# Kernel optimization log

Hardware: AMD Instinct MI355X
Metric: run time of the kernel (lower is better)

The kernel has to match this reference:

```python
import jax, jax.numpy as jnp
import numpy as np

N, E, C, A, F = 10000, 128000, 128, 10, 8
LDIMS = (1, 3, 5)  # 0e, 1o, 2e spherical-harmonic block sizes
NPATH = len(LDIMS)


def setup_inputs() -> dict:
    key = jax.random.key(0)
    ks = jax.random.split(key, 16)
    rn = lambda k, s, sc=1.0: jax.random.normal(k, s, dtype=jnp.float32) * sc
    inp = {
        "node_attrs": rn(ks[0], (N, A)),
        "node_feats": rn(ks[1], (N, C)),
        "edge_attrs_real": rn(ks[2], (E, 9)),
        "edge_attrs_imag": rn(ks[3], (E, 9)),
        "edge_feats": jax.random.uniform(ks[4], (E, F), dtype=jnp.float32),
        "edge_index": jax.random.randint(ks[5], (2, E), 0, N, dtype=jnp.int32),
        # learned parameters (e3nn 1/sqrt(fan_in) normalization folded into init)
        "W_up": rn(ks[6], (C, C), 1.0 / np.sqrt(C)),            # o3.Linear on 128x0e
        "W_skip": rn(ks[7], (C, A, C), 1.0 / np.sqrt(C * A)),    # FullyConnectedTensorProduct
        "W_mlp1": rn(ks[8], (F, 64), 1.0 / np.sqrt(F)),
        "W_mlp2": rn(ks[9], (64, 64), 1.0 / 8.0),
        "W_mlp3": rn(ks[10], (64, 64), 1.0 / 8.0),
        "W_mlp4": rn(ks[11], (64, NPATH * C), 1.0 / 8.0),        # -> conv_tp.weight_numel = 384
        "W_lin0": rn(ks[12], (C, C), 1.0 / np.sqrt(C)),          # o3.Linear per-l blocks
        "W_lin1": rn(ks[13], (C, C), 1.0 / np.sqrt(C)),
        "W_lin2": rn(ks[14], (C, C), 1.0 / np.sqrt(C)),
    }
    return inp


def _conv_tp(x, y, w):
    """scalar(128x0e) x sh(0e+1o+2e) uvu tensor product with per-edge weights.
    x: [E,C] sender scalars, y: [E,9] edge sh, w: [E,NPATH,C] -> [E, C*9] irreps_mid layout."""
    outs, off = [], 0
    for l, d in enumerate(LDIMS):
        yl = y[:, off:off + d]                      # [E,d]
        off += d
        xw = x * w[:, l]                            # [E,C]
        outs.append((xw[:, :, None] * yl[:, None, :]).reshape(-1, C * d))
    return jnp.concatenate(outs, axis=-1)           # [E, C*(1+3+5)]


def _linear_irreps(m, Ws):
    """o3.Linear mixing channels within each l block. m: [N, C*9] -> [N, C, 9]."""
    outs, off = [], 0
    for l, d in enumerate(LDIMS):
        blk = m[:, off:off + C * d].reshape(-1, C, d)  # [N,C,d]
        off += C * d
        outs.append(jnp.einsum('num,uk->nkm', blk, Ws[l]))
    return jnp.concatenate(outs, axis=-1)              # [N,C,9] (reshape_irreps layout)


def reference(node_attrs, node_feats, edge_attrs_real, edge_attrs_imag, edge_feats,
              edge_index, W_up, W_skip, W_mlp1, W_mlp2, W_mlp3, W_mlp4,
              W_lin0, W_lin1, W_lin2):
    sender, receiver = edge_index[0], edge_index[1]
    # skip connection: FullyConnectedTensorProduct(node_feats 128x0e, node_attrs 10x0e)
    sc = jnp.einsum('nu,nv,uvk->nk', node_feats, node_attrs, W_skip)
    # linear_up
    h = node_feats @ W_up
    # per-edge tensor-product weights from radial MLP (silu hidden layers, linear out)
    t = jax.nn.silu(edge_feats @ W_mlp1)
    t = jax.nn.silu(t @ W_mlp2)
    t = jax.nn.silu(t @ W_mlp3)
    tpw = (t @ W_mlp4).reshape(-1, NPATH, C)
    # gather senders, tensor product for real and imag edge attrs
    xs = h[sender]
    mji_r = _conv_tp(xs, edge_attrs_real, tpw)
    mji_i = _conv_tp(xs, edge_attrs_imag, tpw)
    # scatter-sum to receivers
    msg_r = jax.ops.segment_sum(mji_r, receiver, num_segments=N)
    msg_i = jax.ops.segment_sum(mji_i, receiver, num_segments=N)
    # output linear + reshape_irreps -> [N, C, 9]
    Ws = (W_lin0, W_lin1, W_lin2)
    out_r = _linear_irreps(msg_r, Ws)
    out_i = _linear_irreps(msg_i, Ws)
    return out_r, out_i, sc
```

## Files before the change

kernel.cpp:

```cpp
#include <hip/hip_runtime.h>
#include <hip/hip_bf16.h>

#define N_NODES 10000
#define N_EDGES 128000
#define C_DIM   128

typedef __attribute__((ext_vector_type(8))) short bf16x8;
typedef __attribute__((ext_vector_type(4))) float f32x4;


__device__ __forceinline__ float silu_f(float x) {
  return x / (1.f + __expf(-x));
}

__device__ __forceinline__ unsigned short f2bf(float x) {
  __hip_bfloat16 b = __float2bfloat16(x);
  return *(unsigned short*)&b;
}

__device__ __forceinline__ float bf2f(unsigned short u) {
  __hip_bfloat16 b = *(__hip_bfloat16*)&u;
  return __bfloat162float(b);
}

__device__ __forceinline__ bf16x8 pack8(float4 lo, float4 hi) {
  bf16x8 r;
  r[0] = (short)f2bf(lo.x); r[1] = (short)f2bf(lo.y);
  r[2] = (short)f2bf(lo.z); r[3] = (short)f2bf(lo.w);
  r[4] = (short)f2bf(hi.x); r[5] = (short)f2bf(hi.y);
  r[6] = (short)f2bf(hi.z); r[7] = (short)f2bf(hi.w);
  return r;
}

#define HB_NODES 40
__global__ __launch_bounds__(256) void k_h(const float* __restrict__ feats,
                                           const float* __restrict__ Wup,
                                           float* __restrict__ h) {
  int tid = threadIdx.x;
  int j = tid & 127;
  int par = tid >> 7;
  int n0 = blockIdx.x * HB_NODES;
  float wreg[128];
  #pragma unroll
  for (int k = 0; k < 128; k++) wreg[k] = Wup[k * 128 + j];
  #pragma unroll 2
  for (int i = par; i < HB_NODES; i += 2) {
    int n = __builtin_amdgcn_readfirstlane(n0 + i);
    const float* fr = &feats[n * 128];
    float acc = 0.f;
    #pragma unroll
    for (int k = 0; k < 128; k++) acc += fr[k] * wreg[k];
    h[n * 128 + j] = acc;
  }
}

__global__ void k_wcvt(const float* __restrict__ Wskip,
                       const float* __restrict__ Wl0,
                       const float* __restrict__ Wl1,
                       const float* __restrict__ Wl2,
                       const float* __restrict__ W1, const float* __restrict__ W2,
                       const float* __restrict__ W3, const float* __restrict__ W4,
                       unsigned short* __restrict__ wbT,
                       unsigned short* __restrict__ wlT,
                       unsigned short* __restrict__ w1f, unsigned short* __restrict__ w2f,
                       unsigned short* __restrict__ w3f, unsigned short* __restrict__ w4f) {
  int idx = blockIdx.x * 256 + threadIdx.x;
  if (idx < 163840) {
    int j = idx >> 7, k = idx & 127;
    int u = j / 10, v = j - u * 10;
    wbT[k * 1280 + v * 128 + u] = f2bf(Wskip[idx]);
  } else if (idx < 212992) {
    int t = idx - 163840;
    int l = t >> 14, r = t & 16383;
    int u = r >> 7, k = r & 127;
    const float* W = (l == 0) ? Wl0 : (l == 1) ? Wl1 : Wl2;
    wlT[(l * 128 + k) * 128 + u] = f2bf(W[r]);
  } else if (idx < 215040) {
    int j = idx - 212992;
    int ct = j >> 9, r = j & 511, n = r >> 5, t = r & 31;
    w1f[j] = (t < 8) ? f2bf(W1[t * 64 + ct * 16 + n]) : (unsigned short)0;
  } else if (idx < 219136) {
    int j = idx - 215040;
    int ctks = j >> 9, r = j & 511, n = r >> 5, t = r & 31;
    int ct = ctks >> 1, ks = ctks & 1;
    w2f[j] = f2bf(W2[(ks * 32 + t) * 64 + ct * 16 + n]);
  } else if (idx < 223232) {
    int j = idx - 219136;
    int ctks = j >> 9, r = j & 511, n = r >> 5, t = r & 31;
    int ct = ctks >> 1, ks = ctks & 1;
    w3f[j] = f2bf(W3[(ks * 32 + t) * 64 + ct * 16 + n]);
  } else if (idx < 247808) {
    int j = idx - 223232;
    int ctks = j >> 9, r = j & 511, n = r >> 5, t = r & 31;
    int ct = ctks >> 1, ks = ctks & 1;
    w4f[j] = f2bf(W4[(ks * 32 + t) * 384 + ct * 16 + n]);
  }
}

__global__ __launch_bounds__(256) void k_sc(const float* __restrict__ f,
                                            const float* __restrict__ at,
                                            const unsigned short* __restrict__ wbT,
                                            float* __restrict__ sc_out) {
  int tid = threadIdx.x;
  int w = tid >> 6, lane = tid & 63;
  int l15 = lane & 15, quad = lane >> 4;
  int n0 = blockIdx.x * 32;

  int nrow[2];
  #pragma unroll
  for (int t = 0; t < 2; t++) {
    int n = n0 + 16 * t + l15;
    nrow[t] = (n < N_NODES) ? n : (N_NODES - 1);
  }
  float4 fA[2][4][2];
  #pragma unroll
  for (int t = 0; t < 2; t++)
    #pragma unroll
    for (int ks = 0; ks < 4; ks++) {
      fA[t][ks][0] = *(const float4*)&f[nrow[t] * 128 + ks * 32 + quad * 8];
      fA[t][ks][1] = *(const float4*)&f[nrow[t] * 128 + ks * 32 + quad * 8 + 4];
    }

  f32x4 acc[2][2] = {};
  #pragma unroll 1
  for (int c = 0; c < 10; c++) {
    float av[2];
    #pragma unroll
    for (int t = 0; t < 2; t++) av[t] = at[nrow[t] * 10 + c];
    bf16x8 af[2][4];
    #pragma unroll
    for (int t = 0; t < 2; t++)
      #pragma unroll
      for (int ks = 0; ks < 4; ks++) {
        float4 lo = fA[t][ks][0], hi = fA[t][ks][1];
        lo.x *= av[t]; lo.y *= av[t]; lo.z *= av[t]; lo.w *= av[t];
        hi.x *= av[t]; hi.y *= av[t]; hi.z *= av[t]; hi.w *= av[t];
        af[t][ks] = pack8(lo, hi);
      }
    #pragma unroll
    for (int kt = 0; kt < 2; kt++) {
      int kcol = w * 32 + kt * 16 + l15;
      #pragma unroll
      for (int ks = 0; ks < 4; ks++) {
        bf16x8 bf = *(const bf16x8*)&wbT[kcol * 1280 + c * 128 + ks * 32 + quad * 8];
        #pragma unroll
        for (int t = 0; t < 2; t++)
          acc[t][kt] = __builtin_amdgcn_mfma_f32_16x16x32_bf16(af[t][ks], bf,
                                                               acc[t][kt], 0, 0, 0);
      }
    }
  }
  #pragma unroll
  for (int t = 0; t < 2; t++)
    #pragma unroll
    for (int kt = 0; kt < 2; kt++) {
      int kcol = w * 32 + kt * 16 + l15;
      #pragma unroll
      for (int reg = 0; reg < 4; reg++) {
        int n = n0 + 16 * t + quad * 4 + reg;
        if (n < N_NODES)
          __builtin_nontemporal_store(acc[t][kt][reg], &sc_out[n * 128 + kcol]);
      }
    }
}

__global__ __launch_bounds__(256) void k_mlp(const float* __restrict__ ef,
                                             const int* __restrict__ order,
                                             const unsigned short* __restrict__ w1f,
                                             const unsigned short* __restrict__ w2f,
                                             const unsigned short* __restrict__ w3f,
                                             const unsigned short* __restrict__ w4f,
                                             unsigned short* __restrict__ tpw) {
  __shared__ unsigned short sA[128][72];
  __shared__ unsigned short sB[128][72];
  int tid = threadIdx.x;
  int w = tid >> 6, lane = tid & 63;
  int l15 = lane & 15, quad = lane >> 4;
  int e0 = blockIdx.x * 128;
  int fragoff = l15 * 32 + quad * 8;
  int rb = w * 32;

  {
    bf16x8 af[2];
    #pragma unroll
    for (int rt = 0; rt < 2; rt++) {
      bf16x8 a = {};
      if (quad == 0) {
        int pos = e0 + rb + rt * 16 + l15;
        int e = order[pos];
        float4 lo = *(const float4*)&ef[e * 8];
        float4 hi = *(const float4*)&ef[e * 8 + 4];
        a = pack8(lo, hi);
      }
      af[rt] = a;
    }
    f32x4 ac[2][4] = {};
    #pragma unroll
    for (int ct = 0; ct < 4; ct++) {
      bf16x8 b = *(const bf16x8*)&w1f[ct * 512 + fragoff];
      ac[0][ct] = __builtin_amdgcn_mfma_f32_16x16x32_bf16(af[0], b, ac[0][ct], 0, 0, 0);
      ac[1][ct] = __builtin_amdgcn_mfma_f32_16x16x32_bf16(af[1], b, ac[1][ct], 0, 0, 0);
    }
    #pragma unroll
    for (int rt = 0; rt < 2; rt++)
      #pragma unroll
      for (int ct = 0; ct < 4; ct++)
        #pragma unroll
        for (int reg = 0; reg < 4; reg++)
          sA[rb + rt * 16 + quad * 4 + reg][ct * 16 + l15] =
              f2bf(silu_f(ac[rt][ct][reg]));
  }
  asm volatile("" ::: "memory");

  #pragma unroll 1
  for (int layer = 0; layer < 2; layer++) {
    unsigned short (*src)[72] = (layer == 0) ? sA : sB;
    unsigned short (*dst)[72] = (layer == 0) ? sB : sA;
    const unsigned short* wf = (layer == 0) ? w2f : w3f;
    bf16x8 a2[2][2];
    #pragma unroll
    for (int rt = 0; rt < 2; rt++)
      #pragma unroll
      for (int ks = 0; ks < 2; ks++)
        a2[rt][ks] = *(const bf16x8*)&src[rb + rt * 16 + l15][ks * 32 + quad * 8];
    f32x4 ac[2][4] = {};
    #pragma unroll
    for (int ct = 0; ct < 4; ct++)
      #pragma unroll
      for (int ks = 0; ks < 2; ks++) {
        bf16x8 b = *(const bf16x8*)&wf[(ct * 2 + ks) * 512 + fragoff];
        ac[0][ct] = __builtin_amdgcn_mfma_f32_16x16x32_bf16(a2[0][ks], b, ac[0][ct], 0, 0, 0);
        ac[1][ct] = __builtin_amdgcn_mfma_f32_16x16x32_bf16(a2[1][ks], b, ac[1][ct], 0, 0, 0);
      }
    #pragma unroll
    for (int rt = 0; rt < 2; rt++)
      #pragma unroll
      for (int ct = 0; ct < 4; ct++)
        #pragma unroll
        for (int reg = 0; reg < 4; reg++)
          dst[rb + rt * 16 + quad * 4 + reg][ct * 16 + l15] =
              f2bf(silu_f(ac[rt][ct][reg]));
    asm volatile("" ::: "memory");
  }

  bf16x8 a4[2][2];
  #pragma unroll
  for (int rt = 0; rt < 2; rt++)
    #pragma unroll
    for (int ks = 0; ks < 2; ks++)
      a4[rt][ks] = *(const bf16x8*)&sA[rb + rt * 16 + l15][ks * 32 + quad * 8];

  #pragma unroll 1
  for (int ch = 0; ch < 6; ch++) {
    f32x4 ac[2][4] = {};
    #pragma unroll
    for (int ct = 0; ct < 4; ct++)
      #pragma unroll
      for (int ks = 0; ks < 2; ks++) {
        bf16x8 b = *(const bf16x8*)&w4f[((ch * 4 + ct) * 2 + ks) * 512 + fragoff];
        ac[0][ct] = __builtin_amdgcn_mfma_f32_16x16x32_bf16(a4[0][ks], b, ac[0][ct], 0, 0, 0);
        ac[1][ct] = __builtin_amdgcn_mfma_f32_16x16x32_bf16(a4[1][ks], b, ac[1][ct], 0, 0, 0);
      }
    #pragma unroll
    for (int rt = 0; rt < 2; rt++)
      #pragma unroll
      for (int ct = 0; ct < 4; ct++)
        #pragma unroll
        for (int reg = 0; reg < 4; reg++)
          sB[rb + rt * 16 + quad * 4 + reg][ct * 16 + l15] = f2bf(ac[rt][ct][reg]);
    asm volatile("" ::: "memory");
    #pragma unroll
    for (int v = 0; v < 4; v++) {
      int idx = v * 64 + lane;
      int r = idx >> 3, cg = idx & 7;
      uint4 p = *(const uint4*)&sB[rb + r][cg * 8];
      *(uint4*)&tpw[(size_t)(e0 + rb + r) * 384 + ch * 64 + cg * 8] = p;
    }
    asm volatile("" ::: "memory");
  }
}

__global__ void k_hist(const int* __restrict__ recv, int* __restrict__ counts) {
  int e = blockIdx.x * 256 + threadIdx.x;
  if (e < N_EDGES) atomicAdd(&counts[recv[e]], 1);
}

__global__ __launch_bounds__(1024) void k_scan(const int* __restrict__ counts,
                                               int* __restrict__ offsets,
                                               int* __restrict__ cursor) {
  __shared__ int swave[16];
  int tid = threadIdx.x;
  int lane = tid & 63, w = tid >> 6;
  int base = tid * 10;
  int local[10]; int s = 0;
  #pragma unroll
  for (int i = 0; i < 10; i++) {
    int idx = base + i;
    int c = (idx < N_NODES) ? counts[idx] : 0;
    local[i] = s; s += c;
  }
  int inc = s;
  #pragma unroll
  for (int d = 1; d < 64; d <<= 1) {
    int v = __shfl_up(inc, d, 64);
    if (lane >= d) inc += v;
  }
  if (lane == 63) swave[w] = inc;
  __syncthreads();
  if (w == 0) {
    int t = (lane < 16) ? swave[lane] : 0;
    #pragma unroll
    for (int d = 1; d < 16; d <<= 1) {
      int v = __shfl_up(t, d, 64);
      if (lane >= d) t += v;
    }
    if (lane < 16) swave[lane] = t;
  }
  __syncthreads();
  int wpre = (w > 0) ? swave[w - 1] : 0;
  int pre = wpre + (inc - s);
  #pragma unroll
  for (int i = 0; i < 10; i++) {
    int idx = base + i;
    if (idx < N_NODES) { int o = pre + local[i]; offsets[idx] = o; cursor[idx] = o; }
  }
  if (tid == 1023) offsets[N_NODES] = wpre + inc;
}

__global__ void k_scatter(const int* __restrict__ recv, const int* __restrict__ send,
                          const float* __restrict__ yr, const float* __restrict__ yi,
                          int* __restrict__ cursor, int* __restrict__ order,
                          float* __restrict__ y2, int* __restrict__ ss) {
  int e = blockIdx.x * 256 + threadIdx.x;
  if (e < N_EDGES) {
    int idx = atomicAdd(&cursor[recv[e]], 1);
    order[idx] = e;
    ss[idx] = send[e];
    float* yy = &y2[(size_t)idx * 20];
    #pragma unroll
    for (int m = 0; m < 9; m++) {
      yy[m] = yr[e * 9 + m];
      yy[9 + m] = yi[e * 9 + m];
    }
    yy[18] = 0.f; yy[19] = 0.f;
  }
}

__device__ __forceinline__ void edge_fma(const float* __restrict__ y2, int pos,
                                         float xv, float t0, float t1, float t2,
                                         float* mr, float* mi) {
  const float* yy = &y2[(size_t)pos * 20];
  float4 v0 = *(const float4*)&yy[0];
  float4 v1 = *(const float4*)&yy[4];
  float4 v2 = *(const float4*)&yy[8];
  float4 v3 = *(const float4*)&yy[12];
  float2 v4 = *(const float2*)&yy[16];
  float xw0 = xv * t0, xw1 = xv * t1, xw2 = xv * t2;
  mr[0] += xw0 * v0.x;
  mr[1] += xw1 * v0.y; mr[2] += xw1 * v0.z; mr[3] += xw1 * v0.w;
  mr[4] += xw2 * v1.x; mr[5] += xw2 * v1.y; mr[6] += xw2 * v1.z;
  mr[7] += xw2 * v1.w; mr[8] += xw2 * v2.x;
  mi[0] += xw0 * v2.y;
  mi[1] += xw1 * v2.z; mi[2] += xw1 * v2.w; mi[3] += xw1 * v3.x;
  mi[4] += xw2 * v3.y; mi[5] += xw2 * v3.z; mi[6] += xw2 * v3.w;
  mi[7] += xw2 * v4.x; mi[8] += xw2 * v4.y;
}

__global__ __launch_bounds__(128, 6) void k_gather(
    const float* __restrict__ h, const unsigned short* __restrict__ tpw,
    const float* __restrict__ y2, const int* __restrict__ ss,
    const int* __restrict__ offsets,
    unsigned short* __restrict__ msg) {
  int u = threadIdx.x;
  int n = blockIdx.x;
  float mr[9] = {}, mi[9] = {};
  int e0 = __builtin_amdgcn_readfirstlane(offsets[n]);
  int e1 = __builtin_amdgcn_readfirstlane(offsets[n + 1]);
  int jj = e0;
  for (; jj + 3 < e1; jj += 4) {
    float xv[4], t0[4], t1[4], t2[4];
    #pragma unroll
    for (int q = 0; q < 4; q++) {
      int pos = jj + q;
      int s = ss[pos];
      const unsigned short* tp = &tpw[(size_t)pos * 384 + u];
      t0[q] = bf2f(__builtin_nontemporal_load(tp));
      t1[q] = bf2f(__builtin_nontemporal_load(tp + 128));
      t2[q] = bf2f(__builtin_nontemporal_load(tp + 256));
      xv[q] = h[s * 128 + u];
    }
    #pragma unroll
    for (int q = 0; q < 4; q++)
      edge_fma(y2, jj + q, xv[q], t0[q], t1[q], t2[q], mr, mi);
  }
  for (; jj < e1; jj++) {
    int s = ss[jj];
    const unsigned short* tp = &tpw[(size_t)jj * 384 + u];
    float t0 = bf2f(__builtin_nontemporal_load(tp));
    float t1 = bf2f(__builtin_nontemporal_load(tp + 128));
    float t2 = bf2f(__builtin_nontemporal_load(tp + 256));
    float xv = h[s * 128 + u];
    edge_fma(y2, jj, xv, t0, t1, t2, mr, mi);
  }
  int g = n >> 3, i = n & 7;
  unsigned short* mg = msg + (size_t)g * 144 * 128;
  mg[(i * 2 + 0) * 128 + u] = f2bf(mr[0]);
  mg[(i * 2 + 1) * 128 + u] = f2bf(mi[0]);
  #pragma unroll
  for (int m = 1; m < 4; m++) {
    mg[(16 + i * 6 + (m - 1)) * 128 + u] = f2bf(mr[m]);
    mg[(16 + i * 6 + 3 + (m - 1)) * 128 + u] = f2bf(mi[m]);
  }
  #pragma unroll
  for (int m = 4; m < 9; m++) {
    mg[(64 + i * 10 + (m - 4)) * 128 + u] = f2bf(mr[m]);
    mg[(64 + i * 10 + 5 + (m - 4)) * 128 + u] = f2bf(mi[m]);
  }
}

#define LIN_ROWPAD 1156
__global__ __launch_bounds__(256) void k_lin(const unsigned short* __restrict__ msg,
                                             const unsigned short* __restrict__ wlT,
                                             float* __restrict__ out) {
  __shared__ float so[2 * 8 * LIN_ROWPAD];
  int tid = threadIdx.x;
  int w = tid >> 6, lane = tid & 63;
  int l15 = lane & 15, quad = lane >> 4;
  int g = blockIdx.x;

  bf16x8 bfr[3][2][4];
  #pragma unroll
  for (int l = 0; l < 3; l++)
    #pragma unroll
    for (int kt = 0; kt < 2; kt++)
      #pragma unroll
      for (int ks = 0; ks < 4; ks++) {
        int ncol = w * 32 + kt * 16 + l15;
        bfr[l][kt][ks] = *(const bf16x8*)&wlT[(l * 128 + ncol) * 128 + ks * 32 + quad * 8];
      }

  const unsigned short* mg = msg + (size_t)g * 144 * 128;

  #pragma unroll
  for (int tile = 0; tile < 9; tile++) {
    const int l = (tile == 0) ? 0 : (tile < 4) ? 1 : 2;
    const int rbase = tile * 16;
    bf16x8 af[4];
    #pragma unroll
    for (int ks = 0; ks < 4; ks++)
      af[ks] = *(const bf16x8*)&mg[(rbase + l15) * 128 + ks * 32 + quad * 8];
    f32x4 acc0 = {}, acc1 = {};
    #pragma unroll
    for (int ks = 0; ks < 4; ks++) {
      acc0 = __builtin_amdgcn_mfma_f32_16x16x32_bf16(af[ks], bfr[l][0][ks], acc0, 0, 0, 0);
      acc1 = __builtin_amdgcn_mfma_f32_16x16x32_bf16(af[ks], bfr[l][1][ks], acc1, 0, 0, 0);
    }
    #pragma unroll
    for (int reg = 0; reg < 4; reg++) {
      int r = rbase + quad * 4 + reg;
      int c, ni, m;
      if (tile == 0) { ni = (r & 15) >> 1; c = r & 1; m = 0; }
      else if (tile < 4) {
        int q = r - 16; ni = q / 6; int rem = q - ni * 6;
        c = rem >= 3; m = 1 + rem - (c ? 3 : 0);
      } else {
        int q = r - 64; ni = q / 10; int rem = q - ni * 10;
        c = rem >= 5; m = 4 + rem - (c ? 5 : 0);
      }
      int k0 = w * 32 + l15;
      float* ob = &so[(c * 8 + ni) * LIN_ROWPAD + m];
      ob[(k0)      * 9] = acc0[reg];
      ob[(k0 + 16) * 9] = acc1[reg];
    }
  }
  __syncthreads();
  #pragma unroll
  for (int v = 0; v < 18; v++) {
    int idx = v * 256 + tid;
    int c = idx / 2304;
    int rem = idx - c * 2304;
    int ni = rem / 288;
    int off4 = rem - ni * 288;
    f32x4 p = *(const f32x4*)&so[(c * 8 + ni) * LIN_ROWPAD + off4 * 4];
    f32x4* dst = (f32x4*)&out[(size_t)c * 11520000 + ((size_t)g * 8 + ni) * 1152 +
                              (size_t)off4 * 4];
    __builtin_nontemporal_store(p, dst);
  }
}

extern "C" void kernel_launch(void* const* d_in, const int* in_sizes, int n_in,
                              void* d_out, int out_size, void* d_ws, size_t ws_size,
                              hipStream_t stream) {
  const float* node_attrs = (const float*)d_in[0];
  const float* node_feats = (const float*)d_in[1];
  const float* ear   = (const float*)d_in[2];
  const float* eai   = (const float*)d_in[3];
  const float* ef    = (const float*)d_in[4];
  const int*   eidx  = (const int*)d_in[5];
  const float* Wup   = (const float*)d_in[6];
  const float* Wskip = (const float*)d_in[7];
  const float* W1    = (const float*)d_in[8];
  const float* W2    = (const float*)d_in[9];
  const float* W3    = (const float*)d_in[10];
  const float* W4    = (const float*)d_in[11];
  const float* Wl0   = (const float*)d_in[12];
  const float* Wl1   = (const float*)d_in[13];
  const float* Wl2   = (const float*)d_in[14];
  float* out = (float*)d_out;

  char* ws = (char*)d_ws;
  float*          h       = (float*)ws;
  unsigned short* tpw     = (unsigned short*)(ws + 5120000);
  unsigned short* msg     = (unsigned short*)(ws + 103424000);
  unsigned short* wlT     = (unsigned short*)(ws + 149504000);
  unsigned short* wbT     = (unsigned short*)(ws + 149602304);
  int*            counts  = (int*)(ws + 149929984);
  int*            offsets = (int*)(ws + 149969984);
  int*            cursor  = (int*)(ws + 150010112);
  int*            order   = (int*)(ws + 150050112);
  unsigned short* w1f     = (unsigned short*)(ws + 150562816);
  unsigned short* w2f     = (unsigned short*)(ws + 150566912);
  unsigned short* w3f     = (unsigned short*)(ws + 150575104);
  unsigned short* w4f     = (unsigned short*)(ws + 150583296);

  float* y2 = (float*)d_out;
  int*   ss = (int*)((char*)d_out + 10240000);

  const int* send = eidx;
  const int* recv = eidx + N_EDGES;

  hipMemsetAsync(counts, 0, N_NODES * sizeof(int), stream);
  k_hist<<<dim3(500), dim3(256), 0, stream>>>(recv, counts);
  k_scan<<<dim3(1), dim3(1024), 0, stream>>>(counts, offsets, cursor);
  k_scatter<<<dim3(500), dim3(256), 0, stream>>>(recv, send, ear, eai, cursor,
                                                 order, y2, ss);
  k_wcvt<<<dim3(968), dim3(256), 0, stream>>>(Wskip, Wl0, Wl1, Wl2,
                                              W1, W2, W3, W4,
                                              wbT, wlT, w1f, w2f, w3f, w4f);
  k_h<<<dim3(250), dim3(256), 0, stream>>>(node_feats, Wup, h);
  k_sc<<<dim3(313), dim3(256), 0, stream>>>(node_feats, node_attrs, wbT,
                                            out + 2 * 11520000);
  k_mlp<<<dim3(1000), dim3(256), 0, stream>>>(ef, order, w1f, w2f, w3f, w4f, tpw);
  k_gather<<<dim3(10000), dim3(128), 0, stream>>>(h, tpw, y2, ss, offsets, msg);
  k_lin<<<dim3(1250), dim3(256), 0, stream>>>(msg, wlT, out);
  (void)in_sizes; (void)n_in; (void)out_size; (void)ws_size;
}
```

Before: 333.3 us.

## Merge independent prep kernels into two block-dispatched fat kernels

Combines scatter, weight conversion and the h linear into one launch whose block ranges select the role, and likewise merges the skip-connection MFMA kernel with the radial MLP kernel. The skip kernel now handles 16 nodes per block instead of 32. The goal is to cut launch overheads and let independent work overlap on the GPU instead of running serially. In exchange, the fat kernels take on the register and LDS footprint of their heaviest branch (k_h holds 128 weights in registers, the MLP uses shared buffers), which may reduce occupancy for the lighter roles.

```diff
diff --git a/kernel.cpp b/kernel.cpp
--- a/kernel.cpp
+++ b/kernel.cpp
@@ -32,151 +32,194 @@
   return r;
 }
 
+__global__ void k_hist(const int* __restrict__ recv, int* __restrict__ counts) {
+  int e = blockIdx.x * 256 + threadIdx.x;
+  if (e < N_EDGES) atomicAdd(&counts[recv[e]], 1);
+}
+
+__global__ __launch_bounds__(1024) void k_scan(const int* __restrict__ counts,
+                                               int* __restrict__ offsets,
+                                               int* __restrict__ cursor) {
+  __shared__ int swave[16];
+  int tid = threadIdx.x;
+  int lane = tid & 63, w = tid >> 6;
+  int base = tid * 10;
+  int local[10]; int s = 0;
+  #pragma unroll
+  for (int i = 0; i < 10; i++) {
+    int idx = base + i;
+    int c = (idx < N_NODES) ? counts[idx] : 0;
+    local[i] = s; s += c;
+  }
+  int inc = s;
+  #pragma unroll
+  for (int d = 1; d < 64; d <<= 1) {
+    int v = __shfl_up(inc, d, 64);
+    if (lane >= d) inc += v;
+  }
+  if (lane == 63) swave[w] = inc;
+  __syncthreads();
+  if (w == 0) {
+    int t = (lane < 16) ? swave[lane] : 0;
+    #pragma unroll
+    for (int d = 1; d < 16; d <<= 1) {
+      int v = __shfl_up(t, d, 64);
+      if (lane >= d) t += v;
+    }
+    if (lane < 16) swave[lane] = t;
+  }
+  __syncthreads();
+  int wpre = (w > 0) ? swave[w - 1] : 0;
+  int pre = wpre + (inc - s);
+  #pragma unroll
+  for (int i = 0; i < 10; i++) {
+    int idx = base + i;
+    if (idx < N_NODES) { int o = pre + local[i]; offsets[idx] = o; cursor[idx] = o; }
+  }
+  if (tid == 1023) offsets[N_NODES] = wpre + inc;
+}
+
 #define HB_NODES 40
-__global__ __launch_bounds__(256) void k_h(const float* __restrict__ feats,
-                                           const float* __restrict__ Wup,
-                                           float* __restrict__ h) {
+__global__ __launch_bounds__(256) void k_fat1(
+    const int* __restrict__ recv, const int* __restrict__ send,
+    const float* __restrict__ yr, const float* __restrict__ yi,
+    int* __restrict__ cursor, int* __restrict__ order,
+    float* __restrict__ y2, int* __restrict__ ss,
+    const float* __restrict__ Wskip,
+    const float* __restrict__ Wl0, const float* __restrict__ Wl1,
+    const float* __restrict__ Wl2,
+    const float* __restrict__ W1, const float* __restrict__ W2,
+    const float* __restrict__ W3, const float* __restrict__ W4,
+    unsigned short* __restrict__ wbT, unsigned short* __restrict__ wlT,
+    unsigned short* __restrict__ w1f, unsigned short* __restrict__ w2f,
+    unsigned short* __restrict__ w3f, unsigned short* __restrict__ w4f,
+    const float* __restrict__ feats, const float* __restrict__ Wup,
+    float* __restrict__ h) {
+  int b = blockIdx.x;
   int tid = threadIdx.x;
-  int j = tid & 127;
-  int par = tid >> 7;
-  int n0 = blockIdx.x * HB_NODES;
-  float wreg[128];
-  #pragma unroll
-  for (int k = 0; k < 128; k++) wreg[k] = Wup[k * 128 + j];
-  #pragma unroll 2
-  for (int i = par; i < HB_NODES; i += 2) {
-    int n = __builtin_amdgcn_readfirstlane(n0 + i);
-    const float* fr = &feats[n * 128];
-    float acc = 0.f;
-    #pragma unroll
-    for (int k = 0; k < 128; k++) acc += fr[k] * wreg[k];
-    h[n * 128 + j] = acc;
-  }
-}
-
-__global__ void k_wcvt(const float* __restrict__ Wskip,
-                       const float* __restrict__ Wl0,
-                       const float* __restrict__ Wl1,
-                       const float* __restrict__ Wl2,
-                       const float* __restrict__ W1, const float* __restrict__ W2,
-                       const float* __restrict__ W3, const float* __restrict__ W4,
-                       unsigned short* __restrict__ wbT,
-                       unsigned short* __restrict__ wlT,
-                       unsigned short* __restrict__ w1f, unsigned short* __restrict__ w2f,
-                       unsigned short* __restrict__ w3f, unsigned short* __restrict__ w4f) {
-  int idx = blockIdx.x * 256 + threadIdx.x;
-  if (idx < 163840) {
-    int j = idx >> 7, k = idx & 127;
-    int u = j / 10, v = j - u * 10;
-    wbT[k * 1280 + v * 128 + u] = f2bf(Wskip[idx]);
-  } else if (idx < 212992) {
-    int t = idx - 163840;
-    int l = t >> 14, r = t & 16383;
-    int u = r >> 7, k = r & 127;
-    const float* W = (l == 0) ? Wl0 : (l == 1) ? Wl1 : Wl2;
-    wlT[(l * 128 + k) * 128 + u] = f2bf(W[r]);
-  } else if (idx < 215040) {
-    int j = idx - 212992;
-    int ct = j >> 9, r = j & 511, n = r >> 5, t = r & 31;
-    w1f[j] = (t < 8) ? f2bf(W1[t * 64 + ct * 16 + n]) : (unsigned short)0;
-  } else if (idx < 219136) {
-    int j = idx - 215040;
-    int ctks = j >> 9, r = j & 511, n = r >> 5, t = r & 31;
-    int ct = ctks >> 1, ks = ctks & 1;
-    w2f[j] = f2bf(W2[(ks * 32 + t) * 64 + ct * 16 + n]);
-  } else if (idx < 223232) {
-    int j = idx - 219136;
-    int ctks = j >> 9, r = j & 511, n = r >> 5, t = r & 31;
-    int ct = ctks >> 1, ks = ctks & 1;
-    w3f[j] = f2bf(W3[(ks * 32 + t) * 64 + ct * 16 + n]);
-  } else if (idx < 247808) {
-    int j = idx - 223232;
-    int ctks = j >> 9, r = j & 511, n = r >> 5, t = r & 31;
-    int ct = ctks >> 1, ks = ctks & 1;
-    w4f[j] = f2bf(W4[(ks * 32 + t) * 384 + ct * 16 + n]);
-  }
-}
-
-__global__ __launch_bounds__(256) void k_sc(const float* __restrict__ f,
-                                            const float* __restrict__ at,
-                                            const unsigned short* __restrict__ wbT,
-                                            float* __restrict__ sc_out) {
+  if (b < 500) {
+    int e = b * 256 + tid;
+    if (e < N_EDGES) {
+      int idx = atomicAdd(&cursor[recv[e]], 1);
+      order[idx] = e;
+      ss[idx] = send[e];
+      float* yy = &y2[(size_t)idx * 20];
+      #pragma unroll
+      for (int m = 0; m < 9; m++) {
+        yy[m] = yr[e * 9 + m];
+        yy[9 + m] = yi[e * 9 + m];
+      }
+      yy[18] = 0.f; yy[19] = 0.f;
+    }
+  } else if (b < 1468) {
+    int idx = (b - 500) * 256 + tid;
+    if (idx < 163840) {
+      int j = idx >> 7, k = idx & 127;
+      int u = j / 10, v = j - u * 10;
+      wbT[k * 1280 + v * 128 + u] = f2bf(Wskip[idx]);
+    } else if (idx < 212992) {
+      int t = idx - 163840;
+      int l = t >> 14, r = t & 16383;
+      int u = r >> 7, k = r & 127;
+      const float* W = (l == 0) ? Wl0 : (l == 1) ? Wl1 : Wl2;
+      wlT[(l * 128 + k) * 128 + u] = f2bf(W[r]);
+    } else if (idx < 215040) {
+      int j = idx - 212992;
+      int ct = j >> 9, r = j & 511, n = r >> 5, t = r & 31;
+      w1f[j] = (t < 8) ? f2bf(W1[t * 64 + ct * 16 + n]) : (unsigned short)0;
+    } else if (idx < 219136) {
+      int j = idx - 215040;
+      int ctks = j >> 9, r = j & 511, n = r >> 5, t = r & 31;
+      int ct = ctks >> 1, ks = ctks & 1;
+      w2f[j] = f2bf(W2[(ks * 32 + t) * 64 + ct * 16 + n]);
+    } else if (idx < 223232) {
+      int j = idx - 219136;
+      int ctks = j >> 9, r = j & 511, n = r >> 5, t = r & 31;
+      int ct = ctks >> 1, ks = ctks & 1;
+      w3f[j] = f2bf(W3[(ks * 32 + t) * 64 + ct * 16 + n]);
+    } else if (idx < 247808) {
+      int j = idx - 223232;
+      int ctks = j >> 9, r = j & 511, n = r >> 5, t = r & 31;
+      int ct = ctks >> 1, ks = ctks & 1;
+      w4f[j] = f2bf(W4[(ks * 32 + t) * 384 + ct * 16 + n]);
+    }
+  } else {
+    int j = tid & 127;
+    int par = tid >> 7;
+    int n0 = (b - 1468) * HB_NODES;
+    float wreg[128];
+    #pragma unroll
+    for (int k = 0; k < 128; k++) wreg[k] = Wup[k * 128 + j];
+    #pragma unroll 2
+    for (int i = par; i < HB_NODES; i += 2) {
+      int n = __builtin_amdgcn_readfirstlane(n0 + i);
+      const float* fr = &feats[n * 128];
+      float acc = 0.f;
+      #pragma unroll
+      for (int k = 0; k < 128; k++) acc += fr[k] * wreg[k];
+      h[n * 128 + j] = acc;
+    }
+  }
+}
+
+__global__ __launch_bounds__(256) void k_fat2(
+    const float* __restrict__ f, const float* __restrict__ at,
+    const unsigned short* __restrict__ wbT, float* __restrict__ sc_out,
+    const float* __restrict__ ef, const int* __restrict__ order,
+    const unsigned short* __restrict__ w1f, const unsigned short* __restrict__ w2f,
+    const unsigned short* __restrict__ w3f, const unsigned short* __restrict__ w4f,
+    unsigned short* __restrict__ tpw) {
+  __shared__ unsigned short sA[128][72];
+  __shared__ unsigned short sB[128][72];
+  int b = blockIdx.x;
   int tid = threadIdx.x;
   int w = tid >> 6, lane = tid & 63;
   int l15 = lane & 15, quad = lane >> 4;
-  int n0 = blockIdx.x * 32;
-
-  int nrow[2];
-  #pragma unroll
-  for (int t = 0; t < 2; t++) {
-    int n = n0 + 16 * t + l15;
-    nrow[t] = (n < N_NODES) ? n : (N_NODES - 1);
-  }
-  float4 fA[2][4][2];
-  #pragma unroll
-  for (int t = 0; t < 2; t++)
+
+  if (b < 625) {
+    int n0 = b * 16;
+    int nrow = n0 + l15;
+    float4 fA[4][2];
     #pragma unroll
     for (int ks = 0; ks < 4; ks++) {
-      fA[t][ks][0] = *(const float4*)&f[nrow[t] * 128 + ks * 32 + quad * 8];
-      fA[t][ks][1] = *(const float4*)&f[nrow[t] * 128 + ks * 32 + quad * 8 + 4];
-    }
-
-  f32x4 acc[2][2] = {};
-  #pragma unroll 1
-  for (int c = 0; c < 10; c++) {
-    float av[2];
-    #pragma unroll
-    for (int t = 0; t < 2; t++) av[t] = at[nrow[t] * 10 + c];
-    bf16x8 af[2][4];
-    #pragma unroll
-    for (int t = 0; t < 2; t++)
+      fA[ks][0] = *(const float4*)&f[nrow * 128 + ks * 32 + quad * 8];
+      fA[ks][1] = *(const float4*)&f[nrow * 128 + ks * 32 + quad * 8 + 4];
+    }
+    f32x4 acc[2] = {};
+    #pragma unroll 1
+    for (int c = 0; c < 10; c++) {
+      float av = at[nrow * 10 + c];
+      bf16x8 af[4];
       #pragma unroll
       for (int ks = 0; ks < 4; ks++) {
-        float4 lo = fA[t][ks][0], hi = fA[t][ks][1];
-        lo.x *= av[t]; lo.y *= av[t]; lo.z *= av[t]; lo.w *= av[t];
-        hi.x *= av[t]; hi.y *= av[t]; hi.z *= av[t]; hi.w *= av[t];
-        af[t][ks] = pack8(lo, hi);
-      }
+        float4 lo = fA[ks][0], hi = fA[ks][1];
+        lo.x *= av; lo.y *= av; lo.z *= av; lo.w *= av;
+        hi.x *= av; hi.y *= av; hi.z *= av; hi.w *= av;
+        af[ks] = pack8(lo, hi);
+      }
+      #pragma unroll
+      for (int kt = 0; kt < 2; kt++) {
+        int kcol = w * 32 + kt * 16 + l15;
+        #pragma unroll
+        for (int ks = 0; ks < 4; ks++) {
+          bf16x8 bf = *(const bf16x8*)&wbT[kcol * 1280 + c * 128 + ks * 32 + quad * 8];
+          acc[kt] = __builtin_amdgcn_mfma_f32_16x16x32_bf16(af[ks], bf, acc[kt], 0, 0, 0);
+        }
+      }
+    }
     #pragma unroll
     for (int kt = 0; kt < 2; kt++) {
       int kcol = w * 32 + kt * 16 + l15;
       #pragma unroll
-      for (int ks = 0; ks < 4; ks++) {
-        bf16x8 bf = *(const bf16x8*)&wbT[kcol * 1280 + c * 128 + ks * 32 + quad * 8];
-        #pragma unroll
-        for (int t = 0; t < 2; t++)
-          acc[t][kt] = __builtin_amdgcn_mfma_f32_16x16x32_bf16(af[t][ks], bf,
-                                                               acc[t][kt], 0, 0, 0);
-      }
-    }
-  }
-  #pragma unroll
-  for (int t = 0; t < 2; t++)
-    #pragma unroll
-    for (int kt = 0; kt < 2; kt++) {
-      int kcol = w * 32 + kt * 16 + l15;
-      #pragma unroll
       for (int reg = 0; reg < 4; reg++) {
-        int n = n0 + 16 * t + quad * 4 + reg;
-        if (n < N_NODES)
-          __builtin_nontemporal_store(acc[t][kt][reg], &sc_out[n * 128 + kcol]);
-      }
-    }
-}
-
-__global__ __launch_bounds__(256) void k_mlp(const float* __restrict__ ef,
-                                             const int* __restrict__ order,
-                                             const unsigned short* __restrict__ w1f,
-                                             const unsigned short* __restrict__ w2f,
-                                             const unsigned short* __restrict__ w3f,
-                                             const unsigned short* __restrict__ w4f,
-                                             unsigned short* __restrict__ tpw) {
-  __shared__ unsigned short sA[128][72];
-  __shared__ unsigned short sB[128][72];
-  int tid = threadIdx.x;
-  int w = tid >> 6, lane = tid & 63;
-  int l15 = lane & 15, quad = lane >> 4;
-  int e0 = blockIdx.x * 128;
+        int n = n0 + quad * 4 + reg;
+        __builtin_nontemporal_store(acc[kt][reg], &sc_out[n * 128 + kcol]);
+      }
+    }
+    return;
+  }
+
+  int e0 = (b - 625) * 128;
   int fragoff = l15 * 32 + quad * 8;
   int rb = w * 32;
 
@@ -197,9 +240,9 @@
     f32x4 ac[2][4] = {};
     #pragma unroll
     for (int ct = 0; ct < 4; ct++) {
-      bf16x8 b = *(const bf16x8*)&w1f[ct * 512 + fragoff];
-      ac[0][ct] = __builtin_amdgcn_mfma_f32_16x16x32_bf16(af[0], b, ac[0][ct], 0, 0, 0);
-      ac[1][ct] = __builtin_amdgcn_mfma_f32_16x16x32_bf16(af[1], b, ac[1][ct], 0, 0, 0);
+      bf16x8 bb = *(const bf16x8*)&w1f[ct * 512 + fragoff];
+      ac[0][ct] = __builtin_amdgcn_mfma_f32_16x16x32_bf16(af[0], bb, ac[0][ct], 0, 0, 0);
+      ac[1][ct] = __builtin_amdgcn_mfma_f32_16x16x32_bf16(af[1], bb, ac[1][ct], 0, 0, 0);
     }
     #pragma unroll
     for (int rt = 0; rt < 2; rt++)
@@ -228,9 +271,9 @@
     for (int ct = 0; ct < 4; ct++)
       #pragma unroll
       for (int ks = 0; ks < 2; ks++) {
-        bf16x8 b = *(const bf16x8*)&wf[(ct * 2 + ks) * 512 + fragoff];
-        ac[0][ct] = __builtin_amdgcn_mfma_f32_16x16x32_bf16(a2[0][ks], b, ac[0][ct], 0, 0, 0);
-        ac[1][ct] = __builtin_amdgcn_mfma_f32_16x16x32_bf16(a2[1][ks], b, ac[1][ct], 0, 0, 0);
+        bf16x8 bb = *(const bf16x8*)&wf[(ct * 2 + ks) * 512 + fragoff];
+        ac[0][ct] = __builtin_amdgcn_mfma_f32_16x16x32_bf16(a2[0][ks], bb, ac[0][ct], 0, 0, 0);
+        ac[1][ct] = __builtin_amdgcn_mfma_f32_16x16x32_bf16(a2[1][ks], bb, ac[1][ct], 0, 0, 0);
       }
     #pragma unroll
     for (int rt = 0; rt < 2; rt++)
@@ -257,9 +300,9 @@
     for (int ct = 0; ct < 4; ct++)
       #pragma unroll
       for (int ks = 0; ks < 2; ks++) {
-        bf16x8 b = *(const bf16x8*)&w4f[((ch * 4 + ct) * 2 + ks) * 512 + fragoff];
-        ac[0][ct] = __builtin_amdgcn_mfma_f32_16x16x32_bf16(a4[0][ks], b, ac[0][ct], 0, 0, 0);
-        ac[1][ct] = __builtin_amdgcn_mfma_f32_16x16x32_bf16(a4[1][ks], b, ac[1][ct], 0, 0, 0);
+        bf16x8 bb = *(const bf16x8*)&w4f[((ch * 4 + ct) * 2 + ks) * 512 + fragoff];
+        ac[0][ct] = __builtin_amdgcn_mfma_f32_16x16x32_bf16(a4[0][ks], bb, ac[0][ct], 0, 0, 0);
+        ac[1][ct] = __builtin_amdgcn_mfma_f32_16x16x32_bf16(a4[1][ks], bb, ac[1][ct], 0, 0, 0);
       }
     #pragma unroll
     for (int rt = 0; rt < 2; rt++)
@@ -277,72 +320,6 @@
       *(uint4*)&tpw[(size_t)(e0 + rb + r) * 384 + ch * 64 + cg * 8] = p;
     }
     asm volatile("" ::: "memory");
-  }
-}
-
-__global__ void k_hist(const int* __restrict__ recv, int* __restrict__ counts) {
-  int e = blockIdx.x * 256 + threadIdx.x;
-  if (e < N_EDGES) atomicAdd(&counts[recv[e]], 1);
-}
-
-__global__ __launch_bounds__(1024) void k_scan(const int* __restrict__ counts,
-                                               int* __restrict__ offsets,
-                                               int* __restrict__ cursor) {
-  __shared__ int swave[16];
-  int tid = threadIdx.x;
-  int lane = tid & 63, w = tid >> 6;
-  int base = tid * 10;
-  int local[10]; int s = 0;
-  #pragma unroll
-  for (int i = 0; i < 10; i++) {
-    int idx = base + i;
-    int c = (idx < N_NODES) ? counts[idx] : 0;
-    local[i] = s; s += c;
-  }
-  int inc = s;
-  #pragma unroll
-  for (int d = 1; d < 64; d <<= 1) {
-    int v = __shfl_up(inc, d, 64);
-    if (lane >= d) inc += v;
-  }
-  if (lane == 63) swave[w] = inc;
-  __syncthreads();
-  if (w == 0) {
-    int t = (lane < 16) ? swave[lane] : 0;
-    #pragma unroll
-    for (int d = 1; d < 16; d <<= 1) {
-      int v = __shfl_up(t, d, 64);
-      if (lane >= d) t += v;
-    }
-    if (lane < 16) swave[lane] = t;
-  }
-  __syncthreads();
-  int wpre = (w > 0) ? swave[w - 1] : 0;
-  int pre = wpre + (inc - s);
-  #pragma unroll
-  for (int i = 0; i < 10; i++) {
-    int idx = base + i;
-    if (idx < N_NODES) { int o = pre + local[i]; offsets[idx] = o; cursor[idx] = o; }
-  }
-  if (tid == 1023) offsets[N_NODES] = wpre + inc;
-}
-
-__global__ void k_scatter(const int* __restrict__ recv, const int* __restrict__ send,
-                          const float* __restrict__ yr, const float* __restrict__ yi,
-                          int* __restrict__ cursor, int* __restrict__ order,
-                          float* __restrict__ y2, int* __restrict__ ss) {
-  int e = blockIdx.x * 256 + threadIdx.x;
-  if (e < N_EDGES) {
-    int idx = atomicAdd(&cursor[recv[e]], 1);
-    order[idx] = e;
-    ss[idx] = send[e];
-    float* yy = &y2[(size_t)idx * 20];
-    #pragma unroll
-    for (int m = 0; m < 9; m++) {
-      yy[m] = yr[e * 9 + m];
-      yy[9 + m] = yi[e * 9 + m];
-    }
-    yy[18] = 0.f; yy[19] = 0.f;
   }
 }
 
@@ -532,15 +509,14 @@
   hipMemsetAsync(counts, 0, N_NODES * sizeof(int), stream);
   k_hist<<<dim3(500), dim3(256), 0, stream>>>(recv, counts);
   k_scan<<<dim3(1), dim3(1024), 0, stream>>>(counts, offsets, cursor);
-  k_scatter<<<dim3(500), dim3(256), 0, stream>>>(recv, send, ear, eai, cursor,
-                                                 order, y2, ss);
-  k_wcvt<<<dim3(968), dim3(256), 0, stream>>>(Wskip, Wl0, Wl1, Wl2,
-                                              W1, W2, W3, W4,
-                                              wbT, wlT, w1f, w2f, w3f, w4f);
-  k_h<<<dim3(250), dim3(256), 0, stream>>>(node_feats, Wup, h);
-  k_sc<<<dim3(313), dim3(256), 0, stream>>>(node_feats, node_attrs, wbT,
-                                            out + 2 * 11520000);
-  k_mlp<<<dim3(1000), dim3(256), 0, stream>>>(ef, order, w1f, w2f, w3f, w4f, tpw);
+  k_fat1<<<dim3(1718), dim3(256), 0, stream>>>(
+      recv, send, ear, eai, cursor, order, y2, ss,
+      Wskip, Wl0, Wl1, Wl2, W1, W2, W3, W4,
+      wbT, wlT, w1f, w2f, w3f, w4f,
+      node_feats, Wup, h);
+  k_fat2<<<dim3(1625), dim3(256), 0, stream>>>(
+      node_feats, node_attrs, wbT, out + 2 * 11520000,
+      ef, order, w1f, w2f, w3f, w4f, tpw);
   k_gather<<<dim3(10000), dim3(128), 0, stream>>>(h, tpw, y2, ss, offsets, msg);
   k_lin<<<dim3(1250), dim3(256), 0, stream>>>(msg, wlT, out);
   (void)in_sizes; (void)n_in; (void)out_size; (void)ws_size;
```

New measurement: 334.3 us. About the same (+0.3%).
